# Kernel optimization log

Measured on AMD Instinct MI355X. Metric: run time of the kernel, lower is better.

## Reference

```python
import jax, jax.numpy as jnp
import numpy as np

D = 1024
H = 16
HD = D // H
T = 2048
B = 2


def layer_norm(x, g, b, eps=1e-5):
    mu = jnp.mean(x, axis=-1, keepdims=True)
    var = jnp.var(x, axis=-1, keepdims=True)
    return (x - mu) * jax.lax.rsqrt(var + eps) * g + b


def setup_inputs() -> dict:
    key = jax.random.key(0)
    ks = jax.random.split(key, 8)
    s = 1.0 / np.sqrt(D)
    return {
        "x": jax.random.normal(ks[0], (B, T, D), dtype=jnp.float32),
        "ln1_g": jnp.ones((D,), jnp.float32),
        "ln1_b": jnp.zeros((D,), jnp.float32),
        "Wq": jax.random.uniform(ks[1], (D, D), jnp.float32, -s, s),
        "Wk": jax.random.uniform(ks[2], (D, D), jnp.float32, -s, s),
        "Wv": jax.random.uniform(ks[3], (D, D), jnp.float32, -s, s),
        "Wo": jax.random.uniform(ks[4], (D, D), jnp.float32, -s, s),
        "ln2_g": jnp.ones((D,), jnp.float32),
        "ln2_b": jnp.zeros((D,), jnp.float32),
        "W1": jax.random.uniform(ks[5], (D, 2 * D), jnp.float32, -s, s),
        "b1": jnp.zeros((2 * D,), jnp.float32),
        "W2": jax.random.uniform(ks[6], (2 * D, D), jnp.float32, -1.0 / np.sqrt(2 * D), 1.0 / np.sqrt(2 * D)),
        "b2": jnp.zeros((D,), jnp.float32),
    }


def reference(x, ln1_g, ln1_b, Wq, Wk, Wv, Wo, ln2_g, ln2_b, W1, b1, W2, b2):
    Bx, Tx, Dx = x.shape
    shortcut = x
    h = layer_norm(x, ln1_g, ln1_b)
    # projections -> [B, H, T, HD]
    q = (h @ Wq).reshape(Bx, Tx, H, HD).transpose(0, 2, 1, 3)
    k = (h @ Wk).reshape(Bx, Tx, H, HD).transpose(0, 2, 1, 3)
    v = (h @ Wv).reshape(Bx, Tx, H, HD).transpose(0, 2, 1, 3)
    scores = jnp.einsum("bhqd,bhkd->bhqk", q, k)  # [B,H,T,T]
    causal = jnp.triu(jnp.ones((Tx, Tx), bool), k=1)
    scores = jnp.where(causal, -jnp.inf, scores)
    attn = jax.nn.softmax(scores / np.sqrt(HD), axis=-1)
    ctx = jnp.einsum("bhqk,bhkd->bhqd", attn, v)
    ctx = ctx.transpose(0, 2, 1, 3).reshape(Bx, Tx, Dx)
    h = ctx @ Wo
    x = h + shortcut
    shortcut = x
    h = layer_norm(x, ln2_g, ln2_b)
    h = jax.nn.gelu(h @ W1 + b1, approximate=False) @ W2 + b2
    return h + shortcut
```

## Files before the change

### kernel.cpp

```cpp
#include <hip/hip_runtime.h>
#include <hip/hip_bf16.h>

typedef __attribute__((ext_vector_type(8))) short short8;
typedef __attribute__((ext_vector_type(4))) float floatx4;
typedef __attribute__((ext_vector_type(4))) unsigned int uintx4;

#define D_MODEL 1024
#define T_SEQ   2048
#define N_HEAD  16
#define NEG_BIG (-1e30f)
#define LDSP 40
#define VP 72
#define PP 72

static __device__ __forceinline__ float bf2f(ushort u) {
  unsigned int x = ((unsigned int)u) << 16;
  return __builtin_bit_cast(float, x);
}
static __device__ __forceinline__ ushort san(ushort u) {
  return ((u & 0x7F80u) == 0x7F80u) ? (ushort)0 : u;
}
static __device__ __forceinline__ float bf2f_s(ushort u) { return bf2f(san(u)); }
static __device__ __forceinline__ ushort f2bf(float f) {
  unsigned int x = __builtin_bit_cast(unsigned int, f);
  x += 0x7FFFu + ((x >> 16) & 1u);
  return (ushort)(x >> 16);
}
static __device__ __forceinline__ float ext_ld(const void* p, size_t i, int isbf) {
  return isbf ? bf2f_s(((const ushort*)p)[i]) : ((const float*)p)[i];
}
static __device__ __forceinline__ void gload16(const void* g, void* l) {
  __builtin_amdgcn_global_load_lds(
      (const __attribute__((address_space(1))) void*)g,
      (__attribute__((address_space(3))) void*)l, 16, 0, 0);
}
static __device__ __forceinline__ void barrier_lds_only() {
  asm volatile("s_waitcnt lgkmcnt(0)" ::: "memory");
  __builtin_amdgcn_s_barrier();
  __builtin_amdgcn_sched_barrier(0);
}

__global__ void detect_dtype(const ushort* x, uint* flag) {
  int tid = threadIdx.x;
  int cnt = 0;
  for (int j = 0; j < 16; j++) {
    ushort u = x[2 * (tid * 16 + j)];
    int e = (u >> 7) & 0xFF;
    if (e >= 0x60 && e <= 0x8F) cnt++;
  }
  for (int d = 32; d; d >>= 1) cnt += __shfl_xor(cnt, d, 64);
  __shared__ int c[4];
  if ((tid & 63) == 0) c[tid >> 6] = cnt;
  __syncthreads();
  if (tid == 0) flag[0] = (c[0] + c[1] + c[2] + c[3] >= 2048) ? 1u : 0u;
}

__global__ __launch_bounds__(256) void prep_all(
    const void* __restrict__ Wq, const void* __restrict__ Wk,
    const void* __restrict__ Wv, const void* __restrict__ Wo,
    const void* __restrict__ W1, const void* __restrict__ W2,
    ushort* __restrict__ oq, ushort* __restrict__ ok, ushort* __restrict__ ov,
    ushort* __restrict__ oo, ushort* __restrict__ o1, ushort* __restrict__ o2,
    const void* __restrict__ x, const void* __restrict__ ln_g,
    const void* __restrict__ ln_b, ushort* __restrict__ ln_out,
    const uint* __restrict__ flagp) {
  int isbf = (int)*flagp;
  int id = blockIdx.x;
  int tid = threadIdx.x;

  if (id >= 8192) {
    int row = id - 8192;
    size_t ro = (size_t)row * D_MODEL;
    float v[4], gv[4], bv[4];
    if (!isbf) {
      floatx4 xv = *((const floatx4*)((const float*)x + ro) + tid);
#pragma unroll
      for (int i = 0; i < 4; i++) v[i] = xv[i];
    } else {
#pragma unroll
      for (int i = 0; i < 4; i++) v[i] = bf2f_s(((const ushort*)x)[ro + tid * 4 + i]);
    }
    float s = 0.f, sq = 0.f;
#pragma unroll
    for (int i = 0; i < 4; i++) { s += v[i]; sq += v[i] * v[i]; }
#pragma unroll
    for (int d = 32; d; d >>= 1) {
      s += __shfl_xor(s, d, 64);
      sq += __shfl_xor(sq, d, 64);
    }
    __shared__ float red[8];
    int wave = tid >> 6, lane = tid & 63;
    if (lane == 0) { red[wave] = s; red[4 + wave] = sq; }
    __syncthreads();
    s = red[0] + red[1] + red[2] + red[3];
    sq = red[4] + red[5] + red[6] + red[7];
    float mu = s * (1.0f / D_MODEL);
    float var = sq * (1.0f / D_MODEL) - mu * mu;
    float rs = rsqrtf(fmaxf(var, 0.f) + 1e-5f);
    if (!isbf) {
      floatx4 g4 = *((const floatx4*)ln_g + tid);
      floatx4 b4 = *((const floatx4*)ln_b + tid);
#pragma unroll
      for (int i = 0; i < 4; i++) { gv[i] = g4[i]; bv[i] = b4[i]; }
    } else {
#pragma unroll
      for (int i = 0; i < 4; i++) {
        gv[i] = bf2f_s(((const ushort*)ln_g)[tid * 4 + i]);
        bv[i] = bf2f_s(((const ushort*)ln_b)[tid * 4 + i]);
      }
    }
    ushort o4[4];
#pragma unroll
    for (int i = 0; i < 4; i++) o4[i] = f2bf((v[i] - mu) * rs * gv[i] + bv[i]);
    *(uint2*)(ln_out + ro + tid * 4) = *(uint2*)o4;
    return;
  }

  const void* in;
  ushort* out;
  int R, C, local;
  if (id < 4096) {
    int w = id >> 10;
    local = id & 1023;
    R = 1024; C = 1024;
    in  = (w == 0) ? Wq : (w == 1) ? Wk : (w == 2) ? Wv : Wo;
    out = (w == 0) ? oq : (w == 1) ? ok : (w == 2) ? ov : oo;
  } else if (id < 6144) {
    local = id - 4096; R = 1024; C = 2048; in = W1; out = o1;
  } else {
    local = id - 6144; R = 2048; C = 1024; in = W2; out = o2;
  }
  int cb = C >> 5;
  int c0 = (local % cb) * 32, r0 = (local / cb) * 32;
  __shared__ float t[32][33];
  int tx = tid & 31, ty = tid >> 5;
  for (int i = ty; i < 32; i += 8)
    t[i][tx] = ext_ld(in, (size_t)(r0 + i) * C + c0 + tx, isbf);
  __syncthreads();
  for (int i = ty; i < 32; i += 8)
    out[(size_t)(c0 + i) * R + r0 + tx] = f2bf(t[tx][i]);
}

__global__ __launch_bounds__(256) void ln_kernel(
    const void* __restrict__ x, const void* __restrict__ g,
    const void* __restrict__ bb, ushort* __restrict__ out,
    int ext, const uint* __restrict__ flagp) {
  int wbf = (int)*flagp;
  int xbf = ext ? wbf : 1;
  int row = blockIdx.x, tid = threadIdx.x;
  size_t ro = (size_t)row * D_MODEL;
  float v[4], gv[4], bv[4];
  if (!xbf) {
    floatx4 xv = *((const floatx4*)((const float*)x + ro) + tid);
#pragma unroll
    for (int i = 0; i < 4; i++) v[i] = xv[i];
  } else {
#pragma unroll
    for (int i = 0; i < 4; i++) v[i] = bf2f_s(((const ushort*)x)[ro + tid * 4 + i]);
  }
  float s = 0.f, sq = 0.f;
#pragma unroll
  for (int i = 0; i < 4; i++) { s += v[i]; sq += v[i] * v[i]; }
#pragma unroll
  for (int d = 32; d; d >>= 1) {
    s += __shfl_xor(s, d, 64);
    sq += __shfl_xor(sq, d, 64);
  }
  __shared__ float red[8];
  int wave = tid >> 6, lane = tid & 63;
  if (lane == 0) { red[wave] = s; red[4 + wave] = sq; }
  __syncthreads();
  s = red[0] + red[1] + red[2] + red[3];
  sq = red[4] + red[5] + red[6] + red[7];
  float mu = s * (1.0f / D_MODEL);
  float var = sq * (1.0f / D_MODEL) - mu * mu;
  float rs = rsqrtf(fmaxf(var, 0.f) + 1e-5f);
  if (!wbf) {
    floatx4 g4 = *((const floatx4*)g + tid);
    floatx4 b4 = *((const floatx4*)bb + tid);
#pragma unroll
    for (int i = 0; i < 4; i++) { gv[i] = g4[i]; bv[i] = b4[i]; }
  } else {
#pragma unroll
    for (int i = 0; i < 4; i++) {
      gv[i] = bf2f_s(((const ushort*)g)[tid * 4 + i]);
      bv[i] = bf2f_s(((const ushort*)bb)[tid * 4 + i]);
    }
  }
  ushort o4[4];
#pragma unroll
  for (int i = 0; i < 4; i++) o4[i] = f2bf((v[i] - mu) * rs * gv[i] + bv[i]);
  *(uint2*)(out + ro + tid * 4) = *(uint2*)o4;
}

template <int EPI, int SPLIT, int NT, int KSTEP>
__global__ __launch_bounds__(256) void gemm_tt(
    const ushort* __restrict__ A, int lda,
    const ushort* __restrict__ Bt, int ldbt,
    void* __restrict__ C0v, ushort* __restrict__ C1, ushort* __restrict__ C2,
    int ldc,
    const void* __restrict__ bias, size_t biasoff,
    const void* __restrict__ res, int ldr,
    int M, int K, const uint* __restrict__ flagp) {
  __shared__ __align__(16) ushort As[128 * KSTEP];
  __shared__ __align__(16) ushort Bs[NT * KSTEP];
  int isbf = (int)*flagp;
  int tid = threadIdx.x;
  int wave = tid >> 6, lane = tid & 63, lm = lane & 15, quad = lane >> 4;
  int m0 = blockIdx.x * 128, n0 = blockIdx.y * NT;
  constexpr int MR = (NT == 128) ? 4 : 2;
  constexpr int RPW = 512 / KSTEP;
  constexpr int RPC = 4 * RPW;
  constexpr int LPR = KSTEP / 8;
  int wm = (NT == 128) ? (wave >> 1) * 64 : wave * 32;
  int wn = (NT == 128) ? (wave & 1) * 64 : 0;
  floatx4 acc[MR][4] = {};
  int srl = lane / LPR;
  int scl = (lane % LPR) * 8;

  for (int kk = 0; kk < K; kk += KSTEP) {
#pragma unroll
    for (int i = 0; i < 128 / RPC; i++)
      gload16(A + (size_t)(m0 + i * RPC + wave * RPW + srl) * lda + kk + scl,
              &As[(i * RPC + wave * RPW) * KSTEP]);
#pragma unroll
    for (int i = 0; i < NT / RPC; i++)
      gload16(Bt + (size_t)(n0 + i * RPC + wave * RPW + srl) * ldbt + kk + scl,
              &Bs[(i * RPC + wave * RPW) * KSTEP]);
    __syncthreads();
#pragma unroll
    for (int kk2 = 0; kk2 < KSTEP; kk2 += 32) {
      short8 af[MR], bf[4];
#pragma unroll
      for (int i = 0; i < MR; i++)
        af[i] = *(const short8*)&As[(wm + i * 16 + lm) * KSTEP + kk2 + quad * 8];
#pragma unroll
      for (int i = 0; i < 4; i++)
        bf[i] = *(const short8*)&Bs[(wn + i * 16 + lm) * KSTEP + kk2 + quad * 8];
#pragma unroll
      for (int mi = 0; mi < MR; mi++)
#pragma unroll
        for (int ni = 0; ni < 4; ni++)
          acc[mi][ni] = __builtin_amdgcn_mfma_f32_16x16x32_bf16(
              af[mi], bf[ni], acc[mi][ni], 0, 0, 0);
    }
    __syncthreads();
  }

  ushort* Cseg = (ushort*)C0v;
  int colbase = n0;
  if (SPLIT) {
    int seg = n0 >> 10;
    Cseg = (seg == 0) ? (ushort*)C0v : (seg == 1 ? C1 : C2);
    colbase = n0 & 1023;
  }
#pragma unroll
  for (int mi = 0; mi < MR; mi++) {
#pragma unroll
    for (int ni = 0; ni < 4; ni++) {
      int col = colbase + wn + ni * 16 + lm;
#pragma unroll
      for (int r = 0; r < 4; r++) {
        int row = m0 + wm + mi * 16 + quad * 4 + r;
        size_t ci = (size_t)row * ldc + col;
        float v = acc[mi][ni][r];
        if (EPI == 2 || EPI == 5) v += ext_ld(bias, biasoff + col, isbf);
        if (EPI == 1) v += ext_ld(res, (size_t)row * ldr + col, isbf);
        if (EPI == 5) v += bf2f(((const ushort*)res)[(size_t)row * ldr + col]);
        if (EPI == 2) v = 0.5f * v * (1.0f + erff(v * 0.70710678118654752f));
        if (EPI == 5 && !isbf) ((float*)C0v)[ci] = v;
        else                   Cseg[ci] = f2bf(v);
      }
    }
  }
}

template <int EPI, int FINAL>
__global__ __launch_bounds__(256) void gemm_kn(
    const ushort* __restrict__ A, int lda,
    const void* __restrict__ B, int ldb, size_t boff,
    void* __restrict__ C, int ldc,
    const void* __restrict__ bias, size_t biasoff,
    const void* __restrict__ res, int ldr,
    int M, int K, const uint* __restrict__ flagp) {
  __shared__ __align__(16) ushort As[128 * LDSP];
  __shared__ __align__(16) ushort Bs[128 * LDSP];
  int isbf = (int)*flagp;
  int tid = threadIdx.x;
  int wave = tid >> 6, lane = tid & 63, lm = lane & 15, quad = lane >> 4;
  int m0 = blockIdx.x * 128, n0 = blockIdx.y * 128;
  int wm = (wave >> 1) * 64, wn = (wave & 1) * 64;
  floatx4 acc[4][4] = {};
  int sr = tid >> 2;
  int sc = (tid & 3) * 8;
  int bk = tid >> 4;
  int bn8 = (tid & 15) * 8;

  for (int kk = 0; kk < K; kk += 32) {
    uintx4 va0 = *(const uintx4*)(A + (size_t)(m0 + sr) * lda + kk + sc);
    uintx4 va1 = *(const uintx4*)(A + (size_t)(m0 + sr + 64) * lda + kk + sc);
    *(uintx4*)&As[sr * LDSP + sc] = va0;
    *(uintx4*)&As[(sr + 64) * LDSP + sc] = va1;
    if (isbf) {
      const ushort* Bu = (const ushort*)B;
#pragma unroll
      for (int p = 0; p < 2; p++) {
        int krow = bk + p * 16;
        uintx4 raw = *(const uintx4*)(Bu + boff + (size_t)(kk + krow) * ldb + n0 + bn8);
        ushort tmp[8] __attribute__((aligned(16)));
        *(uintx4*)tmp = raw;
#pragma unroll
        for (int i = 0; i < 8; i++) Bs[(bn8 + i) * LDSP + krow] = san(tmp[i]);
      }
    } else {
      const float* Bf = (const float*)B;
#pragma unroll
      for (int p = 0; p < 2; p++) {
        int krow = bk + p * 16;
        const float* src = Bf + boff + (size_t)(kk + krow) * ldb + n0 + bn8;
        floatx4 f0 = *(const floatx4*)src;
        floatx4 f1 = *(const floatx4*)(src + 4);
#pragma unroll
        for (int i = 0; i < 4; i++) {
          Bs[(bn8 + i) * LDSP + krow] = f2bf(f0[i]);
          Bs[(bn8 + 4 + i) * LDSP + krow] = f2bf(f1[i]);
        }
      }
    }
    __syncthreads();
    short8 af[4], bf[4];
#pragma unroll
    for (int i = 0; i < 4; i++)
      af[i] = *(const short8*)&As[(wm + i * 16 + lm) * LDSP + quad * 8];
#pragma unroll
    for (int i = 0; i < 4; i++)
      bf[i] = *(const short8*)&Bs[(wn + i * 16 + lm) * LDSP + quad * 8];
#pragma unroll
    for (int mi = 0; mi < 4; mi++)
#pragma unroll
      for (int ni = 0; ni < 4; ni++)
        acc[mi][ni] = __builtin_amdgcn_mfma_f32_16x16x32_bf16(
            af[mi], bf[ni], acc[mi][ni], 0, 0, 0);
    __syncthreads();
  }

#pragma unroll
  for (int mi = 0; mi < 4; mi++) {
#pragma unroll
    for (int ni = 0; ni < 4; ni++) {
      int col = n0 + wn + ni * 16 + lm;
#pragma unroll
      for (int r = 0; r < 4; r++) {
        int row = m0 + wm + mi * 16 + quad * 4 + r;
        size_t ci = (size_t)row * ldc + col;
        float v = acc[mi][ni][r];
        if (EPI == 4)
          v += (FINAL && !isbf) ? ((const float*)C)[ci] : bf2f(((const ushort*)C)[ci]);
        if (EPI == 2 || EPI == 4) v += ext_ld(bias, biasoff + col, isbf);
        if (EPI == 1) v += ext_ld(res, (size_t)row * ldr + col, isbf);
        if (EPI == 4) v += bf2f(((const ushort*)res)[(size_t)row * ldr + col]);
        if (EPI == 2) v = 0.5f * v * (1.0f + erff(v * 0.70710678118654752f));
        if (FINAL && !isbf) ((float*)C)[ci] = v;
        else                ((ushort*)C)[ci] = f2bf(v);
      }
    }
  }
}

__global__ __launch_bounds__(256) void attn_kernel(
    const ushort* __restrict__ q, const ushort* __restrict__ k,
    const ushort* __restrict__ v, ushort* __restrict__ ctx) {
  int tid = threadIdx.x, wave = tid >> 6, lane = tid & 63;
  int lm = lane & 15, quad = lane >> 4;
  int bx = blockIdx.x, h = blockIdx.y, b = blockIdx.z;
  size_t base = (size_t)b * T_SEQ * D_MODEL + h * 64;

  __shared__ __align__(16) ushort Vst[64 * VP];
  __shared__ __align__(16) ushort PlAll[4][16 * PP];
  ushort* Pl = PlAll[wave];

  int vr_r = tid & 63, vcg = (tid >> 6) * 16;
  const ushort* vrow = v + base + vcg;

#pragma unroll
  for (int qsel = 0; qsel < 2; ++qsel) {
    int qt = qsel ? (31 - bx) : bx;
    int qw = qt * 64 + wave * 16;

    short8 aq0 = *(const short8*)&q[base + (size_t)(qw + lm) * D_MODEL + quad * 8];
    short8 aq1 = *(const short8*)&q[base + (size_t)(qw + lm) * D_MODEL + 32 + quad * 8];

    floatx4 O[4] = {};
    float mrq = NEG_BIG, lrq = 0.f;

    int ntiles = qt + 1;

    uintx4 vv0 = *(const uintx4*)(vrow + (size_t)vr_r * D_MODEL);
    uintx4 vv1 = *(const uintx4*)(vrow + (size_t)vr_r * D_MODEL + 8);
    short8 kfa[4], kfb[4];
#pragma unroll
    for (int g = 0; g < 4; g++) {
      const ushort* kr = &k[base + (size_t)(g * 16 + lm) * D_MODEL + quad * 8];
      kfa[g] = *(const short8*)kr;
      kfb[g] = *(const short8*)(kr + 32);
    }

    for (int kt = 0; kt < ntiles; ++kt) {
      int k0 = kt * 64;
      {
        ushort t0[8] __attribute__((aligned(16)));
        ushort t1[8] __attribute__((aligned(16)));
        *(uintx4*)t0 = vv0;
        *(uintx4*)t1 = vv1;
#pragma unroll
        for (int i = 0; i < 8; i++) {
          Vst[(vcg + i) * VP + vr_r] = t0[i];
          Vst[(vcg + 8 + i) * VP + vr_r] = t1[i];
        }
      }
      floatx4 sc[4];
#pragma unroll
      for (int g = 0; g < 4; g++) {
        floatx4 z = {};
        sc[g] = __builtin_amdgcn_mfma_f32_16x16x32_bf16(kfa[g], aq0, z, 0, 0, 0);
        sc[g] = __builtin_amdgcn_mfma_f32_16x16x32_bf16(kfb[g], aq1, sc[g], 0, 0, 0);
      }
      int k0n = (kt + 1 < ntiles) ? k0 + 64 : k0;
      uintx4 nv0 = *(const uintx4*)(vrow + (size_t)(k0n + vr_r) * D_MODEL);
      uintx4 nv1 = *(const uintx4*)(vrow + (size_t)(k0n + vr_r) * D_MODEL + 8);
      short8 nka[4], nkb[4];
#pragma unroll
      for (int g = 0; g < 4; g++) {
        const ushort* kr = &k[base + (size_t)(k0n + g * 16 + lm) * D_MODEL + quad * 8];
        nka[g] = *(const short8*)kr;
        nkb[g] = *(const short8*)(kr + 32);
      }
      bool full = (k0 + 63 <= qw);
      int qrow = qw + lm;
      float a[16];
#pragma unroll
      for (int g = 0; g < 4; g++)
#pragma unroll
        for (int r = 0; r < 4; r++) {
          float s = sc[g][r] * 0.125f;
          if (!full && (k0 + g * 16 + quad * 4 + r > qrow)) s = NEG_BIG;
          a[g * 4 + r] = s;
        }
      float m0 = fmaxf(fmaxf(a[0], a[1]), fmaxf(a[2], a[3]));
      float m1 = fmaxf(fmaxf(a[4], a[5]), fmaxf(a[6], a[7]));
      float m2 = fmaxf(fmaxf(a[8], a[9]), fmaxf(a[10], a[11]));
      float m3 = fmaxf(fmaxf(a[12], a[13]), fmaxf(a[14], a[15]));
      float tm = fmaxf(fmaxf(m0, m1), fmaxf(m2, m3));
      tm = fmaxf(tm, __shfl_xor(tm, 16, 64));
      tm = fmaxf(tm, __shfl_xor(tm, 32, 64));
      float mn = fmaxf(mrq, tm);
      float alpha = __expf(mrq - mn);
      float rs0 = 0.f, rs1 = 0.f;
#pragma unroll
      for (int i = 0; i < 8; i++) { a[i] = __expf(a[i] - mn); rs0 += a[i]; }
#pragma unroll
      for (int i = 8; i < 16; i++) { a[i] = __expf(a[i] - mn); rs1 += a[i]; }
      float rsum = rs0 + rs1;
      rsum += __shfl_xor(rsum, 16, 64);
      rsum += __shfl_xor(rsum, 32, 64);
      mrq = mn;
      lrq = lrq * alpha + rsum;
#pragma unroll
      for (int r = 0; r < 4; r++) {
        float aw = __shfl(alpha, quad * 4 + r, 64);
        O[0][r] *= aw; O[1][r] *= aw; O[2][r] *= aw; O[3][r] *= aw;
      }
#pragma unroll
      for (int g = 0; g < 4; g++) {
        ushort o4[4] __attribute__((aligned(8)));
#pragma unroll
        for (int r = 0; r < 4; r++) o4[r] = f2bf(a[g * 4 + r]);
        *(uint2*)&Pl[lm * PP + g * 16 + quad * 4] = *(uint2*)o4;
      }
      barrier_lds_only();
      short8 pa0 = *(const short8*)&Pl[lm * PP + quad * 8];
      short8 pa1 = *(const short8*)&Pl[lm * PP + 32 + quad * 8];
#pragma unroll
      for (int d4 = 0; d4 < 4; d4++) {
        short8 bv0 = *(const short8*)&Vst[(d4 * 16 + lm) * VP + quad * 8];
        short8 bv1 = *(const short8*)&Vst[(d4 * 16 + lm) * VP + 32 + quad * 8];
        O[d4] = __builtin_amdgcn_mfma_f32_16x16x32_bf16(pa0, bv0, O[d4], 0, 0, 0);
        O[d4] = __builtin_amdgcn_mfma_f32_16x16x32_bf16(pa1, bv1, O[d4], 0, 0, 0);
      }
      barrier_lds_only();
      vv0 = nv0; vv1 = nv1;
#pragma unroll
      for (int g = 0; g < 4; g++) { kfa[g] = nka[g]; kfb[g] = nkb[g]; }
    }
    float linv = 1.0f / fmaxf(lrq, 1e-20f);
#pragma unroll
    for (int r = 0; r < 4; r++) {
      float lw = __shfl(linv, quad * 4 + r, 64);
#pragma unroll
      for (int d4 = 0; d4 < 4; d4++) {
        ctx[base + (size_t)(qw + quad * 4 + r) * D_MODEL + d4 * 16 + lm] =
            f2bf(O[d4][r] * lw);
      }
    }
  }
}

extern "C" void kernel_launch(void* const* d_in, const int* in_sizes, int n_in,
                              void* d_out, int out_size, void* d_ws, size_t ws_size,
                              hipStream_t stream) {
  const void* x     = d_in[0];
  const void* ln1_g = d_in[1];
  const void* ln1_b = d_in[2];
  const void* Wq    = d_in[3];
  const void* Wk    = d_in[4];
  const void* Wv    = d_in[5];
  const void* Wo    = d_in[6];
  const void* ln2_g = d_in[7];
  const void* ln2_b = d_in[8];
  const void* W1    = d_in[9];
  const void* b1    = d_in[10];
  const void* W2    = d_in[11];
  const void* b2    = d_in[12];

  const int M = 2 * T_SEQ;
  const size_t MEG = 1024 * 1024;
  ushort* W = (ushort*)d_ws;
  ushort* Abuf = W;
  ushort* kbuf = W + 4 * MEG;
  ushort* vbuf = W + 8 * MEG;
  ushort* qbuf = (ushort*)d_out;

  dim3 blk(256);
  dim3 g18(32, 8);
  dim3 attng(T_SEQ / 128, N_HEAD, 2);

  bool fast = ws_size >= (size_t)40 * MEG + 4096;

  if (fast) {
    ushort* WqkvT = W + 12 * MEG;
    ushort* WoT   = W + 15 * MEG;
    ushort* W1T   = W + 16 * MEG;
    ushort* W2T   = W + 18 * MEG;
    ushort* act   = W + 8 * MEG;
    uint* flag = (uint*)(W + 20 * MEG);

    detect_dtype<<<1, 256, 0, stream>>>((const ushort*)x, flag);

    prep_all<<<dim3(12288), blk, 0, stream>>>(
        Wq, Wk, Wv, Wo, W1, W2,
        WqkvT, WqkvT + 1 * MEG, WqkvT + 2 * MEG, WoT, W1T, W2T,
        x, ln1_g, ln1_b, Abuf, flag);

    gemm_tt<0, 1, 128, 32><<<dim3(32, 24), blk, 0, stream>>>(
        Abuf, 1024, WqkvT, 1024, qbuf, kbuf, vbuf, 1024,
        nullptr, 0, nullptr, 0, M, 1024, flag);

    attn_kernel<<<attng, blk, 0, stream>>>(qbuf, kbuf, vbuf, Abuf);

    gemm_tt<1, 0, 64, 32><<<dim3(32, 16), blk, 0, stream>>>(
        Abuf, 1024, WoT, 1024, kbuf, nullptr, nullptr, 1024,
        nullptr, 0, x, 1024, M, 1024, flag);

    ln_kernel<<<dim3(M), blk, 0, stream>>>(kbuf, ln2_g, ln2_b, Abuf, 0, flag);

    gemm_tt<2, 0, 64, 32><<<dim3(32, 32), blk, 0, stream>>>(
        Abuf, 1024, W1T, 1024, act, nullptr, nullptr, 2048,
        b1, 0, nullptr, 0, M, 1024, flag);
    gemm_tt<5, 0, 64, 32><<<dim3(32, 16), blk, 0, stream>>>(
        act, 2048, W2T, 2048, d_out, nullptr, nullptr, 1024,
        b2, 0, kbuf, 1024, M, 2048, flag);
  } else {
    uint* flag = (uint*)(W + 12 * MEG);
    detect_dtype<<<1, 256, 0, stream>>>((const ushort*)x, flag);
    ln_kernel<<<dim3(M), blk, 0, stream>>>(x, ln1_g, ln1_b, Abuf, 1, flag);
    gemm_kn<0, 0><<<g18, blk, 0, stream>>>(Abuf, 1024, Wq, 1024, 0, qbuf, 1024,
                                           nullptr, 0, nullptr, 0, M, 1024, flag);
    gemm_kn<0, 0><<<g18, blk, 0, stream>>>(Abuf, 1024, Wk, 1024, 0, kbuf, 1024,
                                           nullptr, 0, nullptr, 0, M, 1024, flag);
    gemm_kn<0, 0><<<g18, blk, 0, stream>>>(Abuf, 1024, Wv, 1024, 0, vbuf, 1024,
                                           nullptr, 0, nullptr, 0, M, 1024, flag);
    attn_kernel<<<attng, blk, 0, stream>>>(qbuf, kbuf, vbuf, Abuf);
    gemm_kn<1, 0><<<g18, blk, 0, stream>>>(Abuf, 1024, Wo, 1024, 0, kbuf, 1024,
                                           nullptr, 0, x, 1024, M, 1024, flag);
    ln_kernel<<<dim3(M), blk, 0, stream>>>(kbuf, ln2_g, ln2_b, Abuf, 0, flag);
    gemm_kn<2, 0><<<g18, blk, 0, stream>>>(Abuf, 1024, W1, 2048, 0, vbuf, 1024,
                                           b1, 0, nullptr, 0, M, 1024, flag);
    gemm_kn<0, 1><<<g18, blk, 0, stream>>>(vbuf, 1024, W2, 1024, 0, d_out, 1024,
                                           nullptr, 0, nullptr, 0, M, 1024, flag);
    gemm_kn<2, 0><<<g18, blk, 0, stream>>>(Abuf, 1024, W1, 2048, 1024, vbuf, 1024,
                                           b1, 1024, nullptr, 0, M, 1024, flag);
    gemm_kn<4, 1><<<g18, blk, 0, stream>>>(vbuf, 1024, W2, 1024, (size_t)1024 * 1024,
                                           d_out, 1024, b2, 0, kbuf, 1024, M, 1024, flag);
  }
}
```

Before: 351.9 us.

## Fold softmax scale into Q exponent, enlarge weight transpose tiles, split mask path

Attention now pre-scales Q by 1/8 by subtracting 3 from the bf16 exponent bits, flushing tiny values to signed zero. This removes the per-score multiply, and the full (unmasked) tiles skip the causal-mask compare. The weight-transpose prep kernel moves from 32x32 to 64x64 tiles, cutting its block count and adjusting the grid and layer-norm block offset to match. The exponent trick is exact except for denormal-range values, and the larger LDS tile may lower occupancy of the prep kernel.

Measured after the change: 345.4 us. Within noise of the previous version (-1.8%).

```diff
diff --git a/kernel.cpp b/kernel.cpp
--- a/kernel.cpp
+++ b/kernel.cpp
@@ -28,6 +28,16 @@
 }
 static __device__ __forceinline__ float ext_ld(const void* p, size_t i, int isbf) {
   return isbf ? bf2f_s(((const ushort*)p)[i]) : ((const float*)p)[i];
+}
+static __device__ __forceinline__ short8 qscale8(short8 v) {
+  short8 o;
+#pragma unroll
+  for (int i = 0; i < 8; i++) {
+    ushort u = (ushort)v[i];
+    int e = (u >> 7) & 0xFF;
+    o[i] = (short)((e > 3) ? (ushort)(u - (3 << 7)) : (ushort)(u & 0x8000u));
+  }
+  return o;
 }
 static __device__ __forceinline__ void gload16(const void* g, void* l) {
   __builtin_amdgcn_global_load_lds(
@@ -68,8 +78,8 @@
   int id = blockIdx.x;
   int tid = threadIdx.x;
 
-  if (id >= 8192) {
-    int row = id - 8192;
+  if (id >= 2048) {
+    int row = id - 2048;
     size_t ro = (size_t)row * D_MODEL;
     float v[4], gv[4], bv[4];
     if (!isbf) {
@@ -119,26 +129,26 @@
   const void* in;
   ushort* out;
   int R, C, local;
-  if (id < 4096) {
-    int w = id >> 10;
-    local = id & 1023;
+  if (id < 1024) {
+    int w = id >> 8;
+    local = id & 255;
     R = 1024; C = 1024;
     in  = (w == 0) ? Wq : (w == 1) ? Wk : (w == 2) ? Wv : Wo;
     out = (w == 0) ? oq : (w == 1) ? ok : (w == 2) ? ov : oo;
-  } else if (id < 6144) {
-    local = id - 4096; R = 1024; C = 2048; in = W1; out = o1;
+  } else if (id < 1536) {
+    local = id - 1024; R = 1024; C = 2048; in = W1; out = o1;
   } else {
-    local = id - 6144; R = 2048; C = 1024; in = W2; out = o2;
-  }
-  int cb = C >> 5;
-  int c0 = (local % cb) * 32, r0 = (local / cb) * 32;
-  __shared__ float t[32][33];
-  int tx = tid & 31, ty = tid >> 5;
-  for (int i = ty; i < 32; i += 8)
-    t[i][tx] = ext_ld(in, (size_t)(r0 + i) * C + c0 + tx, isbf);
+    local = id - 1536; R = 2048; C = 1024; in = W2; out = o2;
+  }
+  int cb = C >> 6;
+  int c0 = (local % cb) * 64, r0 = (local / cb) * 64;
+  __shared__ float t[64][65];
+  int cc = tid & 63, ty = tid >> 6;
+  for (int rr = ty; rr < 64; rr += 4)
+    t[rr][cc] = ext_ld(in, (size_t)(r0 + rr) * C + c0 + cc, isbf);
   __syncthreads();
-  for (int i = ty; i < 32; i += 8)
-    out[(size_t)(c0 + i) * R + r0 + tx] = f2bf(t[tx][i]);
+  for (int i = ty; i < 64; i += 4)
+    out[(size_t)(c0 + i) * R + r0 + cc] = f2bf(t[cc][i]);
 }
 
 __global__ __launch_bounds__(256) void ln_kernel(
@@ -387,8 +397,8 @@
     int qt = qsel ? (31 - bx) : bx;
     int qw = qt * 64 + wave * 16;
 
-    short8 aq0 = *(const short8*)&q[base + (size_t)(qw + lm) * D_MODEL + quad * 8];
-    short8 aq1 = *(const short8*)&q[base + (size_t)(qw + lm) * D_MODEL + 32 + quad * 8];
+    short8 aq0 = qscale8(*(const short8*)&q[base + (size_t)(qw + lm) * D_MODEL + quad * 8]);
+    short8 aq1 = qscale8(*(const short8*)&q[base + (size_t)(qw + lm) * D_MODEL + 32 + quad * 8]);
 
     floatx4 O[4] = {};
     float mrq = NEG_BIG, lrq = 0.f;
@@ -436,16 +446,23 @@
         nkb[g] = *(const short8*)(kr + 32);
       }
       bool full = (k0 + 63 <= qw);
-      int qrow = qw + lm;
       float a[16];
-#pragma unroll
-      for (int g = 0; g < 4; g++)
-#pragma unroll
-        for (int r = 0; r < 4; r++) {
-          float s = sc[g][r] * 0.125f;
-          if (!full && (k0 + g * 16 + quad * 4 + r > qrow)) s = NEG_BIG;
-          a[g * 4 + r] = s;
-        }
+      if (full) {
+#pragma unroll
+        for (int g = 0; g < 4; g++)
+#pragma unroll
+          for (int r = 0; r < 4; r++) a[g * 4 + r] = sc[g][r];
+      } else {
+        int qrow = qw + lm;
+#pragma unroll
+        for (int g = 0; g < 4; g++)
+#pragma unroll
+          for (int r = 0; r < 4; r++) {
+            float s = sc[g][r];
+            if (k0 + g * 16 + quad * 4 + r > qrow) s = NEG_BIG;
+            a[g * 4 + r] = s;
+          }
+      }
       float m0 = fmaxf(fmaxf(a[0], a[1]), fmaxf(a[2], a[3]));
       float m1 = fmaxf(fmaxf(a[4], a[5]), fmaxf(a[6], a[7]));
       float m2 = fmaxf(fmaxf(a[8], a[9]), fmaxf(a[10], a[11]));
@@ -546,7 +563,7 @@
 
     detect_dtype<<<1, 256, 0, stream>>>((const ushort*)x, flag);
 
-    prep_all<<<dim3(12288), blk, 0, stream>>>(
+    prep_all<<<dim3(6144), blk, 0, stream>>>(
         Wq, Wk, Wv, Wo, W1, W2,
         WqkvT, WqkvT + 1 * MEG, WqkvT + 2 * MEG, WoT, W1T, W2T,
         x, ln1_g, ln1_b, Abuf, flag);
```
